# Kernel tuning notes

Hardware: AMD Instinct MI355X
Metric: run time of the kernel (lower is better)

Reference implementation:

```python
import jax, jax.numpy as jnp
import numpy as np

IN_FEATURES = 4096
OUT_FEATURES = 4096
NNZ = 838860
BATCH = 512


def setup_inputs() -> dict:
    key = jax.random.key(0)
    kx, kr, kc, kv, kb = jax.random.split(key, 5)
    x = jax.random.normal(kx, (BATCH, IN_FEATURES), dtype=jnp.float32)
    row_idx = jax.random.randint(kr, (NNZ,), 0, OUT_FEATURES, dtype=jnp.int64)
    col_idx = jax.random.randint(kc, (NNZ,), 0, IN_FEATURES, dtype=jnp.int64)
    values = jax.random.normal(kv, (NNZ,), dtype=jnp.float32)
    bias = jax.random.normal(kb, (OUT_FEATURES,), dtype=jnp.float32)
    return {"x": x, "row_idx": row_idx, "col_idx": col_idx,
            "values": values, "bias": bias}


def reference(x, row_idx, col_idx, values, bias):
    # COO sparse linear: y[b, row] += x[b, col] * val, then add bias.
    x_flat = x.reshape(-1, IN_FEATURES)                    # [B, in]
    weighted = x_flat[:, col_idx] * values                 # [B, nnz]
    out = jnp.zeros((x_flat.shape[0], OUT_FEATURES), dtype=x.dtype)
    out = out.at[:, row_idx].add(weighted)                 # scatter-add per row
    out = out + bias
    return out.reshape(x.shape[:-1] + (OUT_FEATURES,))
```

## Files before the change

kernel.cpp:

```cpp
#include <hip/hip_runtime.h>

#define IN_F    4096
#define OUT_F   4096
#define K_DIM   4096
#define NNZ_C   838860
#define BATCH   512
#define BK      32
#define BM      128
#define BN      128
#define NBLK    1024
#define SCAT_BLKS 820
#define CVT_BLKS  (NBLK - SCAT_BLKS)
#define N_CVT   (BATCH * K_DIM / 8)
#define N_RED   (BATCH * OUT_F / 4)

typedef short bf16x8 __attribute__((ext_vector_type(8)));
typedef float f32x4  __attribute__((ext_vector_type(4)));

__device__ __forceinline__ unsigned short f2bf(float f) {
    unsigned u = __float_as_uint(f);
    u += 0x7fffu + ((u >> 16) & 1u);
    return (unsigned short)(u >> 16);
}
__device__ __forceinline__ void gload_lds16(const void* g, void* l) {
    __builtin_amdgcn_global_load_lds(
        (const __attribute__((address_space(1))) unsigned int*)g,
        (__attribute__((address_space(3))) unsigned int*)l, 16, 0, 0);
}
__device__ __forceinline__ void pk_add(unsigned short* W, int r, int c, float v) {
    unsigned idx = (unsigned)r * K_DIM + (unsigned)c;
    unsigned short h = f2bf(v);
    unsigned data = (idx & 1u) ? ((unsigned)h << 16) : (unsigned)h;
    unsigned long long addr = (unsigned long long)(W + (idx & ~1u));
    asm volatile("global_atomic_pk_add_bf16 %0, %1, off"
                 :: "v"(addr), "v"(data) : "memory");
}

__device__ __forceinline__ void grid_bar(int* cnt, int* gen) {
    __syncthreads();
    if (threadIdx.x == 0) {
        __threadfence();
        int g = __hip_atomic_load(gen, __ATOMIC_RELAXED, __HIP_MEMORY_SCOPE_AGENT);
        int v = __hip_atomic_fetch_add(cnt, 1, __ATOMIC_ACQ_REL, __HIP_MEMORY_SCOPE_AGENT);
        if (v == NBLK - 1) {
            __hip_atomic_store(cnt, 0, __ATOMIC_RELAXED, __HIP_MEMORY_SCOPE_AGENT);
            __hip_atomic_fetch_add(gen, 1, __ATOMIC_ACQ_REL, __HIP_MEMORY_SCOPE_AGENT);
        } else {
            while (__hip_atomic_load(gen, __ATOMIC_ACQUIRE, __HIP_MEMORY_SCOPE_AGENT) == g)
                __builtin_amdgcn_s_sleep(2);
        }
    }
    __syncthreads();
}

template <int EPI, int SK>
__device__ __forceinline__ void gemm_body(
    int nt, int mt, int s, int t,
    const unsigned short* __restrict__ Abf,
    const unsigned short* __restrict__ Wbf,
    const float* __restrict__ bias,
    float* __restrict__ out, float* __restrict__ parts,
    unsigned short* As, unsigned short* Bs) {
    const int w = t >> 6, ln = t & 63;
    const int wm = w & 1, wn = w >> 1;
    const int KSs = K_DIM / SK;
    const int ks0 = s * KSs;

    const int srow = w * 16 + (ln >> 2);
    const int scol = (((ln & 3) ^ ((ln >> 3) & 3)) * 8);
    const unsigned short* gA0 = Abf + (size_t)(mt * BM + srow) * K_DIM + ks0 + scol;
    const unsigned short* gA1 = gA0 + (size_t)64 * K_DIM;
    const unsigned short* gB0 = Wbf + (size_t)(nt * BN + srow) * K_DIM + ks0 + scol;
    const unsigned short* gB1 = gB0 + (size_t)64 * K_DIM;
    unsigned short* lA0 = &As[(w * 16) * BK];
    unsigned short* lA1 = &As[(64 + w * 16) * BK];
    unsigned short* lB0 = &Bs[(w * 16) * BK];
    unsigned short* lB1 = &Bs[(64 + w * 16) * BK];

    const int quad = ln >> 4, lanem = ln & 15;
    const int rsw = (quad ^ ((lanem >> 1) & 3)) * 8;
    const unsigned short* rA = &As[(wm * 64 + lanem) * BK + rsw];
    const unsigned short* rB = &Bs[(wn * 64 + lanem) * BK + rsw];

    f32x4 acc[4][4];
#pragma unroll
    for (int mi = 0; mi < 4; ++mi)
#pragma unroll
        for (int ni = 0; ni < 4; ++ni)
            acc[mi][ni] = (f32x4){0.f, 0.f, 0.f, 0.f};

    for (int kt = 0; kt < KSs / BK; ++kt) {
        __syncthreads();
        gload_lds16(gA0 + kt * BK, lA0);
        gload_lds16(gA1 + kt * BK, lA1);
        gload_lds16(gB0 + kt * BK, lB0);
        gload_lds16(gB1 + kt * BK, lB1);
        __syncthreads();

        bf16x8 af[4], bfr[4];
#pragma unroll
        for (int mi = 0; mi < 4; ++mi) af[mi]  = *(const bf16x8*)(rA + mi * 16 * BK);
#pragma unroll
        for (int ni = 0; ni < 4; ++ni) bfr[ni] = *(const bf16x8*)(rB + ni * 16 * BK);
#pragma unroll
        for (int mi = 0; mi < 4; ++mi)
#pragma unroll
            for (int ni = 0; ni < 4; ++ni)
                acc[mi][ni] = __builtin_amdgcn_mfma_f32_16x16x32_bf16(
                    af[mi], bfr[ni], acc[mi][ni], 0, 0, 0);
    }

    const int row0 = mt * BM + wm * 64 + quad * 4;
    const int col0 = nt * BN + wn * 64 + lanem;
    if (EPI == 0) {
        float bv[4];
#pragma unroll
        for (int ni = 0; ni < 4; ++ni) bv[ni] = (s == 0) ? bias[col0 + ni * 16] : 0.f;
        float* dst = (s == 0) ? out : parts + (size_t)(s - 1) * BATCH * OUT_F;
#pragma unroll
        for (int mi = 0; mi < 4; ++mi)
#pragma unroll
            for (int ni = 0; ni < 4; ++ni)
#pragma unroll
                for (int r = 0; r < 4; ++r)
                    dst[(size_t)(row0 + mi * 16 + r) * OUT_F + col0 + ni * 16] =
                        acc[mi][ni][r] + bv[ni];
    } else {
#pragma unroll
        for (int mi = 0; mi < 4; ++mi)
#pragma unroll
            for (int ni = 0; ni < 4; ++ni)
#pragma unroll
                for (int r = 0; r < 4; ++r)
                    atomicAdd(&out[(size_t)(row0 + mi * 16 + r) * OUT_F + col0 + ni * 16],
                              acc[mi][ni][r]);
    }
}

__global__ void __launch_bounds__(256, 4)
fused(const float* __restrict__ x,
      const int* __restrict__ row_idx,
      const int* __restrict__ col_idx,
      const float* __restrict__ values,
      const float* __restrict__ bias,
      float* __restrict__ out,
      int* __restrict__ bar,
      unsigned short* __restrict__ xb,
      unsigned short* __restrict__ W,
      float* __restrict__ parts) {
    __shared__ __align__(16) unsigned short As[BM * BK];
    __shared__ __align__(16) unsigned short Bs[BN * BK];
    const int b = blockIdx.x, t = threadIdx.x;
    const int gtid = b * 256 + t;

    {
        uint4* Wz = (uint4*)W;
#pragma unroll
        for (int j = 0; j < 8; ++j)
            Wz[(size_t)gtid + (size_t)j * (NBLK * 256)] = make_uint4(0, 0, 0, 0);
    }
    grid_bar(bar, bar + 64);

    if (b < SCAT_BLKS) {
        int i = gtid;
        if (i < NNZ_C / 4) {
            int4   r4 = ((const int4*)row_idx)[i];
            int4   c4 = ((const int4*)col_idx)[i];
            float4 v4 = ((const float4*)values)[i];
            pk_add(W, r4.x, c4.x, v4.x);
            pk_add(W, r4.y, c4.y, v4.y);
            pk_add(W, r4.z, c4.z, v4.z);
            pk_add(W, r4.w, c4.w, v4.w);
        }
    } else {
        for (int j = (b - SCAT_BLKS) * 256 + t; j < N_CVT; j += CVT_BLKS * 256) {
            const float4* p = (const float4*)x + (size_t)j * 2;
            float4 a = p[0], bb = p[1];
            union { unsigned short h[8]; bf16x8 v; } u;
            u.h[0] = f2bf(a.x);  u.h[1] = f2bf(a.y);
            u.h[2] = f2bf(a.z);  u.h[3] = f2bf(a.w);
            u.h[4] = f2bf(bb.x); u.h[5] = f2bf(bb.y);
            u.h[6] = f2bf(bb.z); u.h[7] = f2bf(bb.w);
            ((bf16x8*)xb)[j] = u.v;
        }
    }
    grid_bar(bar, bar + 64);

    gemm_body<0, 8>(b & 31, (b >> 5) & 3, b >> 7, t, xb, W, bias, out, parts,
                    As, Bs);
    grid_bar(bar, bar + 64);

#pragma unroll
    for (int j = 0; j < 2; ++j) {
        size_t i = (size_t)gtid + (size_t)j * (NBLK * 256);
        float4 a = ((const float4*)out)[i];
#pragma unroll
        for (int p = 0; p < 7; ++p) {
            float4 v = ((const float4*)(parts + (size_t)p * BATCH * OUT_F))[i];
            a.x += v.x; a.y += v.y; a.z += v.z; a.w += v.w;
        }
        ((float4*)out)[i] = a;
    }
}

#define N_WZ   (OUT_F * K_DIM / 8)
#define N_OUT  (BATCH * OUT_F / 4)
__global__ void prep(const float* __restrict__ x,
                     unsigned short* __restrict__ xb,
                     const float* __restrict__ bias,
                     float* __restrict__ out,
                     uint4* __restrict__ Wz) {
    int i = blockIdx.x * 256 + threadIdx.x;
    if (i < N_WZ) { Wz[i] = make_uint4(0, 0, 0, 0); return; }
    i -= N_WZ;
    if (i < N_CVT) {
        const float4* p = (const float4*)x + (size_t)i * 2;
        float4 a = p[0], b = p[1];
        union { unsigned short h[8]; bf16x8 v; } u;
        u.h[0] = f2bf(a.x); u.h[1] = f2bf(a.y); u.h[2] = f2bf(a.z); u.h[3] = f2bf(a.w);
        u.h[4] = f2bf(b.x); u.h[5] = f2bf(b.y); u.h[6] = f2bf(b.z); u.h[7] = f2bf(b.w);
        ((bf16x8*)xb)[i] = u.v;
        return;
    }
    i -= N_CVT;
    if (i < N_OUT) {
        float4 b = ((const float4*)bias)[i & (OUT_F / 4 - 1)];
        ((float4*)out)[i] = b;
    }
}
__global__ void scatter_pk(const int* __restrict__ row_idx,
                           const int* __restrict__ col_idx,
                           const float* __restrict__ values,
                           unsigned short* __restrict__ W) {
    int i = blockIdx.x * 256 + threadIdx.x;
    if (i >= NNZ_C / 4) return;
    int4   r4 = ((const int4*)row_idx)[i];
    int4   c4 = ((const int4*)col_idx)[i];
    float4 v4 = ((const float4*)values)[i];
    pk_add(W, r4.x, c4.x, v4.x);
    pk_add(W, r4.y, c4.y, v4.y);
    pk_add(W, r4.z, c4.z, v4.z);
    pk_add(W, r4.w, c4.w, v4.w);
}
__global__ void __launch_bounds__(256)
gemm_atomic(const unsigned short* __restrict__ Abf,
            const unsigned short* __restrict__ Wbf,
            const float* __restrict__ bias,
            float* __restrict__ out) {
    __shared__ __align__(16) unsigned short As[BM * BK];
    __shared__ __align__(16) unsigned short Bs[BN * BK];
    gemm_body<1, 4>(blockIdx.x, blockIdx.y, blockIdx.z, threadIdx.x,
                    Abf, Wbf, bias, out, nullptr, As, Bs);
}

extern "C" void kernel_launch(void* const* d_in, const int* in_sizes, int n_in,
                              void* d_out, int out_size, void* d_ws, size_t ws_size,
                              hipStream_t stream) {
    const float* x       = (const float*)d_in[0];
    const int*   row_idx = (const int*)d_in[1];
    const int*   col_idx = (const int*)d_in[2];
    const float* values  = (const float*)d_in[3];
    const float* bias    = (const float*)d_in[4];
    float*       out     = (float*)d_out;

    int* bar = (int*)d_ws;
    unsigned short* xb = (unsigned short*)((char*)d_ws + 256);
    unsigned short* W  = xb + (size_t)BATCH * K_DIM;
    float* parts = (float*)(W + (size_t)OUT_F * K_DIM);
    size_t need = 256 + (size_t)BATCH * K_DIM * 2 + (size_t)OUT_F * K_DIM * 2
                + (size_t)7 * BATCH * OUT_F * 4;

    int maxb = 0;
    hipError_t e = hipOccupancyMaxActiveBlocksPerMultiprocessor(
        &maxb, (const void*)fused, 256, 0);
    bool coop = (e == hipSuccess) && (maxb >= 4) && (ws_size >= need);

    if (coop) {
        hipMemsetAsync(bar, 0, 256, stream);
        fused<<<NBLK, 256, 0, stream>>>(x, row_idx, col_idx, values, bias,
                                        out, bar, xb, W, parts);
    } else {
        prep<<<(N_WZ + N_CVT + N_OUT) / 256, 256, 0, stream>>>(
            x, xb, bias, out, (uint4*)W);
        scatter_pk<<<(NNZ_C / 4 + 255) / 256, 256, 0, stream>>>(
            row_idx, col_idx, values, W);
        gemm_atomic<<<dim3(OUT_F / BN, BATCH / BM, 4), 256, 0, stream>>>(
            xb, W, bias, out);
    }
}
```

Before: 169.4 us.

## Replace atomic scatter with tag-based plain stores and hierarchical grid barrier

```diff
diff --git a/kernel.cpp b/kernel.cpp
--- a/kernel.cpp
+++ b/kernel.cpp
@@ -4,15 +4,15 @@
 #define OUT_F   4096
 #define K_DIM   4096
 #define NNZ_C   838860
+#define NQ      (NNZ_C / 4)
 #define BATCH   512
 #define BK      32
 #define BM      128
 #define BN      128
 #define NBLK    1024
-#define SCAT_BLKS 820
-#define CVT_BLKS  (NBLK - SCAT_BLKS)
+#define GRPS    8
+#define GRP_SZ  (NBLK / GRPS)
 #define N_CVT   (BATCH * K_DIM / 8)
-#define N_RED   (BATCH * OUT_F / 4)
 
 typedef short bf16x8 __attribute__((ext_vector_type(8)));
 typedef float f32x4  __attribute__((ext_vector_type(4)));
@@ -27,8 +27,7 @@
         (const __attribute__((address_space(1))) unsigned int*)g,
         (__attribute__((address_space(3))) unsigned int*)l, 16, 0, 0);
 }
-__device__ __forceinline__ void pk_add(unsigned short* W, int r, int c, float v) {
-    unsigned idx = (unsigned)r * K_DIM + (unsigned)c;
+__device__ __forceinline__ void pk_add(unsigned short* W, unsigned idx, float v) {
     unsigned short h = f2bf(v);
     unsigned data = (idx & 1u) ? ((unsigned)h << 16) : (unsigned)h;
     unsigned long long addr = (unsigned long long)(W + (idx & ~1u));
@@ -36,18 +35,34 @@
                  :: "v"(addr), "v"(data) : "memory");
 }
 
-__device__ __forceinline__ void grid_bar(int* cnt, int* gen) {
+__device__ __forceinline__ void grid_bar(int* bs) {
     __syncthreads();
     if (threadIdx.x == 0) {
+        const int grp = blockIdx.x & (GRPS - 1);
+        int* cnt  = bs + grp * 32;
+        int* gcnt = bs + 256;
+        int* lgen = bs + 320 + grp * 32;
         __threadfence();
-        int g = __hip_atomic_load(gen, __ATOMIC_RELAXED, __HIP_MEMORY_SCOPE_AGENT);
+        int g = __hip_atomic_load(lgen, __ATOMIC_RELAXED, __HIP_MEMORY_SCOPE_AGENT);
         int v = __hip_atomic_fetch_add(cnt, 1, __ATOMIC_ACQ_REL, __HIP_MEMORY_SCOPE_AGENT);
-        if (v == NBLK - 1) {
-            __hip_atomic_store(cnt, 0, __ATOMIC_RELAXED, __HIP_MEMORY_SCOPE_AGENT);
-            __hip_atomic_fetch_add(gen, 1, __ATOMIC_ACQ_REL, __HIP_MEMORY_SCOPE_AGENT);
+        if (v == GRP_SZ - 1) {
+            int w = __hip_atomic_fetch_add(gcnt, 1, __ATOMIC_ACQ_REL, __HIP_MEMORY_SCOPE_AGENT);
+            if (w == GRPS - 1) {
+                __hip_atomic_store(gcnt, 0, __ATOMIC_RELAXED, __HIP_MEMORY_SCOPE_AGENT);
+#pragma unroll
+                for (int j = 0; j < GRPS; ++j)
+                    __hip_atomic_store(bs + j * 32, 0, __ATOMIC_RELAXED, __HIP_MEMORY_SCOPE_AGENT);
+#pragma unroll
+                for (int j = 0; j < GRPS; ++j)
+                    __hip_atomic_fetch_add(bs + 320 + j * 32, 1,
+                                           __ATOMIC_RELEASE, __HIP_MEMORY_SCOPE_AGENT);
+            } else {
+                while (__hip_atomic_load(lgen, __ATOMIC_ACQUIRE, __HIP_MEMORY_SCOPE_AGENT) == g)
+                    __builtin_amdgcn_s_sleep(2);
+            }
         } else {
-            while (__hip_atomic_load(gen, __ATOMIC_ACQUIRE, __HIP_MEMORY_SCOPE_AGENT) == g)
-                __builtin_amdgcn_s_sleep(2);
+            while (__hip_atomic_load(lgen, __ATOMIC_ACQUIRE, __HIP_MEMORY_SCOPE_AGENT) == g)
+                __builtin_amdgcn_s_sleep(4);
         }
     }
     __syncthreads();
@@ -144,9 +159,10 @@
       const float* __restrict__ values,
       const float* __restrict__ bias,
       float* __restrict__ out,
-      int* __restrict__ bar,
+      int* __restrict__ bs,
       unsigned short* __restrict__ xb,
       unsigned short* __restrict__ W,
+      int* __restrict__ T,
       float* __restrict__ parts) {
     __shared__ __align__(16) unsigned short As[BM * BK];
     __shared__ __align__(16) unsigned short Bs[BN * BK];
@@ -158,37 +174,56 @@
 #pragma unroll
         for (int j = 0; j < 8; ++j)
             Wz[(size_t)gtid + (size_t)j * (NBLK * 256)] = make_uint4(0, 0, 0, 0);
-    }
-    grid_bar(bar, bar + 64);
-
-    if (b < SCAT_BLKS) {
-        int i = gtid;
-        if (i < NNZ_C / 4) {
-            int4   r4 = ((const int4*)row_idx)[i];
-            int4   c4 = ((const int4*)col_idx)[i];
-            float4 v4 = ((const float4*)values)[i];
-            pk_add(W, r4.x, c4.x, v4.x);
-            pk_add(W, r4.y, c4.y, v4.y);
-            pk_add(W, r4.z, c4.z, v4.z);
-            pk_add(W, r4.w, c4.w, v4.w);
+        const float4* p = (const float4*)x + (size_t)gtid * 2;
+        float4 a = p[0], bb = p[1];
+        union { unsigned short h[8]; bf16x8 v; } u;
+        u.h[0] = f2bf(a.x);  u.h[1] = f2bf(a.y);
+        u.h[2] = f2bf(a.z);  u.h[3] = f2bf(a.w);
+        u.h[4] = f2bf(bb.x); u.h[5] = f2bf(bb.y);
+        u.h[6] = f2bf(bb.z); u.h[7] = f2bf(bb.w);
+        ((bf16x8*)xb)[gtid] = u.v;
+    }
+    unsigned eidx[4];
+    float    ev[4];
+    bool     have = (gtid < NQ);
+    if (have) {
+        int4   r4 = ((const int4*)row_idx)[gtid];
+        int4   c4 = ((const int4*)col_idx)[gtid];
+        float4 v4 = ((const float4*)values)[gtid];
+        eidx[0] = (unsigned)r4.x * K_DIM + (unsigned)c4.x;  ev[0] = v4.x;
+        eidx[1] = (unsigned)r4.y * K_DIM + (unsigned)c4.y;  ev[1] = v4.y;
+        eidx[2] = (unsigned)r4.z * K_DIM + (unsigned)c4.z;  ev[2] = v4.z;
+        eidx[3] = (unsigned)r4.w * K_DIM + (unsigned)c4.w;  ev[3] = v4.w;
+#pragma unroll
+        for (int j = 0; j < 4; ++j)
+            T[eidx[j]] = 4 * gtid + j;
+    }
+    grid_bar(bs);
+
+    int lose_mask = 0;
+    if (have) {
+#pragma unroll
+        for (int j = 0; j < 4; ++j) {
+            int tag = __hip_atomic_load(&T[eidx[j]], __ATOMIC_RELAXED,
+                                        __HIP_MEMORY_SCOPE_AGENT);
+            if (tag == 4 * gtid + j)
+                W[eidx[j]] = f2bf(ev[j]);
+            else
+                lose_mask |= (1 << j);
         }
-    } else {
-        for (int j = (b - SCAT_BLKS) * 256 + t; j < N_CVT; j += CVT_BLKS * 256) {
-            const float4* p = (const float4*)x + (size_t)j * 2;
-            float4 a = p[0], bb = p[1];
-            union { unsigned short h[8]; bf16x8 v; } u;
-            u.h[0] = f2bf(a.x);  u.h[1] = f2bf(a.y);
-            u.h[2] = f2bf(a.z);  u.h[3] = f2bf(a.w);
-            u.h[4] = f2bf(bb.x); u.h[5] = f2bf(bb.y);
-            u.h[6] = f2bf(bb.z); u.h[7] = f2bf(bb.w);
-            ((bf16x8*)xb)[j] = u.v;
-        }
-    }
-    grid_bar(bar, bar + 64);
+    }
+    grid_bar(bs);
+
+    if (lose_mask) {
+#pragma unroll
+        for (int j = 0; j < 4; ++j)
+            if (lose_mask & (1 << j)) pk_add(W, eidx[j], ev[j]);
+    }
+    grid_bar(bs);
 
     gemm_body<0, 8>(b & 31, (b >> 5) & 3, b >> 7, t, xb, W, bias, out, parts,
                     As, Bs);
-    grid_bar(bar, bar + 64);
+    grid_bar(bs);
 
 #pragma unroll
     for (int j = 0; j < 2; ++j) {
@@ -233,14 +268,14 @@
                            const float* __restrict__ values,
                            unsigned short* __restrict__ W) {
     int i = blockIdx.x * 256 + threadIdx.x;
-    if (i >= NNZ_C / 4) return;
+    if (i >= NQ) return;
     int4   r4 = ((const int4*)row_idx)[i];
     int4   c4 = ((const int4*)col_idx)[i];
     float4 v4 = ((const float4*)values)[i];
-    pk_add(W, r4.x, c4.x, v4.x);
-    pk_add(W, r4.y, c4.y, v4.y);
-    pk_add(W, r4.z, c4.z, v4.z);
-    pk_add(W, r4.w, c4.w, v4.w);
+    pk_add(W, (unsigned)r4.x * K_DIM + (unsigned)c4.x, v4.x);
+    pk_add(W, (unsigned)r4.y * K_DIM + (unsigned)c4.y, v4.y);
+    pk_add(W, (unsigned)r4.z * K_DIM + (unsigned)c4.z, v4.z);
+    pk_add(W, (unsigned)r4.w * K_DIM + (unsigned)c4.w, v4.w);
 }
 __global__ void __launch_bounds__(256)
 gemm_atomic(const unsigned short* __restrict__ Abf,
@@ -263,26 +298,27 @@
     const float* bias    = (const float*)d_in[4];
     float*       out     = (float*)d_out;
 
-    int* bar = (int*)d_ws;
-    unsigned short* xb = (unsigned short*)((char*)d_ws + 256);
-    unsigned short* W  = xb + (size_t)BATCH * K_DIM;
-    float* parts = (float*)(W + (size_t)OUT_F * K_DIM);
-    size_t need = 256 + (size_t)BATCH * K_DIM * 2 + (size_t)OUT_F * K_DIM * 2
-                + (size_t)7 * BATCH * OUT_F * 4;
+    char* p = (char*)d_ws;
+    int* bs = (int*)p;                       p += 4096;
+    unsigned short* xb = (unsigned short*)p; p += (size_t)BATCH * K_DIM * 2;
+    unsigned short* W  = (unsigned short*)p; p += (size_t)OUT_F * K_DIM * 2;
+    int* T = (int*)p;                        p += (size_t)OUT_F * K_DIM * 4;
+    float* parts = (float*)p;                p += (size_t)7 * BATCH * OUT_F * 4;
+    size_t need_full = (size_t)(p - (char*)d_ws);
 
     int maxb = 0;
     hipError_t e = hipOccupancyMaxActiveBlocksPerMultiprocessor(
         &maxb, (const void*)fused, 256, 0);
-    bool coop = (e == hipSuccess) && (maxb >= 4) && (ws_size >= need);
+    bool coop = (e == hipSuccess) && (maxb >= 4) && (ws_size >= need_full);
 
     if (coop) {
-        hipMemsetAsync(bar, 0, 256, stream);
+        hipMemsetAsync(bs, 0, 4096, stream);
         fused<<<NBLK, 256, 0, stream>>>(x, row_idx, col_idx, values, bias,
-                                        out, bar, xb, W, parts);
+                                        out, bs, xb, W, T, parts);
     } else {
         prep<<<(N_WZ + N_CVT + N_OUT) / 256, 256, 0, stream>>>(
             x, xb, bias, out, (uint4*)W);
-        scatter_pk<<<(NNZ_C / 4 + 255) / 256, 256, 0, stream>>>(
+        scatter_pk<<<(NQ + 255) / 256, 256, 0, stream>>>(
             row_idx, col_idx, values, W);
         gemm_atomic<<<dim3(OUT_F / BN, BATCH / BM, 4), 256, 0, stream>>>(
             xb, W, bias, out);
```

Result: no change. 169.0 us (-0.3%).
